# Kernel tuning notes

Hardware: AMD Instinct MI355X
Metric: run time of the kernel (lower is better)

Reference implementation:

```python
import jax, jax.numpy as jnp
import numpy as np

DIM, NHEADS = 1536, 12
HEAD_DIM = DIM // NHEADS  # 128

def _rope_params(max_pos, d):
    inv = 1.0 / (10000.0 ** (np.arange(0, d, 2, dtype=np.float64) / d))
    ang = np.outer(np.arange(max_pos, dtype=np.float64), inv)
    return np.stack([np.cos(ang), np.sin(ang)], -1).astype(np.float32)  # [max_pos, d//2, 2]

def setup_inputs() -> dict:
    key = jax.random.key(0)
    ks = jax.random.split(key, 8)
    B, F, H, W = 1, 3, 30, 52
    L = F * H * W  # 4680
    def w(k):
        return jax.random.normal(k, (DIM, DIM), jnp.float32) * 0.02
    # Wan rope table: head_dim=128 -> segments of real dim 44, 42, 42 (complex 22,21,21)
    freqs = np.concatenate([_rope_params(1024, 44), _rope_params(1024, 42), _rope_params(1024, 42)], axis=1)
    return {
        "x": jax.random.normal(ks[0], (B, L, DIM), jnp.float32),
        "wq": w(ks[1]), "bq": jnp.zeros((DIM,), jnp.float32),
        "wk": w(ks[2]), "bk": jnp.zeros((DIM,), jnp.float32),
        "wv": w(ks[3]), "bv": jnp.zeros((DIM,), jnp.float32),
        "wo": w(ks[4]), "bo": jnp.zeros((DIM,), jnp.float32),
        "gq": jnp.ones((DIM,), jnp.float32),
        "gk": jnp.ones((DIM,), jnp.float32),
        "freqs": jnp.asarray(freqs),                       # [1024, 64, 2] (cos, sin)
        "seq_lens": jnp.array([L], jnp.int64),
        "grid_sizes": jnp.array([[F, H, W]], jnp.int64),
        "F": F, "H": H, "W": W,
        "sink_size": 1, "local_attn_size": 2,
    }

def _rmsnorm(x, g, eps=1e-6):
    xf = x.astype(jnp.float32)
    return xf * jax.lax.rsqrt(jnp.mean(xf * xf, -1, keepdims=True) + eps) * g

def _rope_table(freqs, F, H, W):
    # freqs: [1024, 64, 2]; split complex dims [22, 21, 21] for (t, h, w)
    c = freqs.shape[1]
    s0 = c - 2 * (c // 3)          # 22
    s1 = c // 3                    # 21
    ft = jnp.broadcast_to(freqs[:F, :s0].reshape(F, 1, 1, s0, 2), (F, H, W, s0, 2))
    fh = jnp.broadcast_to(freqs[:H, s0:s0 + s1].reshape(1, H, 1, s1, 2), (F, H, W, s1, 2))
    fw = jnp.broadcast_to(freqs[:W, s0 + s1:].reshape(1, 1, W, s1, 2), (F, H, W, s1, 2))
    return jnp.concatenate([ft, fh, fw], -2).reshape(F * H * W, c, 2)  # [L, c, 2]

def _apply_rope(t, fr):
    # t: [B, L, n, d]; fr: [L, c, 2] with c = d // 2; complex multiply in real arithmetic
    B, L, n, d = t.shape
    c = d // 2
    tr = t.reshape(B, L, n, c, 2)
    a, b = tr[..., 0], tr[..., 1]
    cos = fr[None, :, None, :, 0]
    sin = fr[None, :, None, :, 1]
    out = jnp.stack([a * cos - b * sin, a * sin + b * cos], -1)
    return out.reshape(B, L, n, d)

def reference(x, wq, bq, wk, bk, wv, bv, wo, bo, gq, gk, freqs, seq_lens, grid_sizes,
              F, H, W, sink_size, local_attn_size):
    B, L, dim = x.shape
    n, d = NHEADS, HEAD_DIM
    q = _rmsnorm(x @ wq.T + bq, gq).reshape(B, L, n, d)
    k = _rmsnorm(x @ wk.T + bk, gk).reshape(B, L, n, d)
    v = (x @ wv.T + bv).reshape(B, L, n, d)
    fr = _rope_table(freqs, F, H, W)
    rq = _apply_rope(q, fr)
    rk = _apply_rope(k, fr)
    # sink + causal local-window block mask at frame granularity
    frame = jnp.arange(L) // (H * W)
    fq, fk = frame[:, None], frame[None, :]
    allow = (fk <= fq) & ((fk < sink_size) | (fq - fk < local_attn_size))  # [L, L]
    scores = jnp.einsum('blnd,bmnd->bnlm', rq, rk) / jnp.sqrt(jnp.float32(d))
    scores = jnp.where(allow[None, None], scores, -jnp.inf)
    p = jax.nn.softmax(scores, axis=-1)
    out = jnp.einsum('bnlm,bmnd->blnd', p, v).reshape(B, L, dim)
    return out @ wo.T + bo
```

## Files before the change

### kernel.cpp

```cpp
#include <hip/hip_runtime.h>

#define L_SEQ 4680
#define DIMSZ 1536
#define NHEAD 12
#define HDIM 128
#define FRAME 1560
#define NKT_ALL 74
#define SCALE_L2E 0.12751743f
#define WSZ 2359296
#define XSZ 7274496
#define PMPITCH 4736

typedef float f32x4 __attribute__((ext_vector_type(4)));
typedef _Float16 f16;
typedef _Float16 f16x2 __attribute__((ext_vector_type(2)));
typedef _Float16 f16x4 __attribute__((ext_vector_type(4)));
typedef _Float16 f16x8 __attribute__((ext_vector_type(8)));
typedef unsigned short u16;

__device__ __forceinline__ void gll16(const void* g, void* l) {
  __builtin_amdgcn_global_load_lds(
      (const __attribute__((address_space(1))) unsigned int*)g,
      (__attribute__((address_space(3))) unsigned int*)l, 16, 0, 0);
}

__global__ __launch_bounds__(256) void split_all(
    const float* __restrict__ x,  const float* __restrict__ wq,
    const float* __restrict__ wk, const float* __restrict__ wv,
    const float* __restrict__ wo, f16* __restrict__ xs,
    f16* __restrict__ whi) {
  const int kt = blockIdx.x;
  const int y = blockIdx.y;
  const float* src; f16* dst; int R, rt;
  if (y < 37) { src = x; dst = xs; R = L_SEQ; rt = y; }
  else {
    int i = y - 37;
    int z = i / 12; rt = i - z * 12; R = DIMSZ;
    src = z == 0 ? wq : (z == 1 ? wk : (z == 2 ? wv : wo));
    dst = whi + (size_t)z * WSZ;
  }
  const int t = threadIdx.x;
  const int row = t >> 1, c0 = (t & 1) * 16;
  const int gr = min(rt * 128 + row, R - 1);
  const float* s = &src[(size_t)gr * DIMSZ + kt * 32 + c0];
  float f[16];
#pragma unroll
  for (int i = 0; i < 4; ++i) *(float4*)&f[i * 4] = *(const float4*)&s[i * 4];
  size_t obase = ((size_t)(rt * 48 + kt)) * 4096 + row * 32;
#pragma unroll
  for (int cc = 0; cc < 2; ++cc) {
    f16x8 o;
#pragma unroll
    for (int i = 0; i < 8; ++i) o[i] = (f16)f[cc * 8 + i];
    int sl = (c0 >> 3) + cc;
    *(f16x8*)&dst[obase + ((sl * 8) ^ ((row & 3) * 8))] = o;
  }
}

__global__ __launch_bounds__(256, 3) void gemm_f16_1p(
    const f16* __restrict__ A, const f16* __restrict__ Wh,
    const float* __restrict__ b0, const float* __restrict__ b1, const float* __restrict__ b2,
    float* __restrict__ C, int M) {
  __shared__ f16 SA[8192];
  __shared__ f16 SW[8192];
  const int t = threadIdx.x;
  const int lane = t & 63, w = t >> 6;
  const int g = lane >> 4, ln = lane & 15;
  const int wm = w >> 1, wn = w & 1;
  const int mt = blockIdx.x, nt = blockIdx.y;
  const int which = nt / 12, ntw = nt - which * 12;
  const float* bias = which == 0 ? b0 : (which == 1 ? b1 : b2);
  const f16* srcA = A + (size_t)mt * 48 * 4096;
  const f16* srcW = Wh + ((size_t)which * 12 + ntw) * 48 * 4096;
  float* Cw = C + (size_t)which * ((size_t)L_SEQ * DIMSZ);
  f32x4 acc[4][4] = {};
  for (int kt2 = 0; kt2 < 24; ++kt2) {
    __syncthreads();
    size_t ko = (size_t)kt2 * 8192;
#pragma unroll
    for (int i = 0; i < 4; ++i) {
      gll16(srcA + ko + (i * 256 + t) * 8, &SA[(i * 256 + t) * 8]);
      gll16(srcW + ko + (i * 256 + t) * 8, &SW[(i * 256 + t) * 8]);
    }
    __syncthreads();
#pragma unroll
    for (int kc = 0; kc < 2; ++kc) {
      f16x8 af[4], wh4[4];
#pragma unroll
      for (int mi = 0; mi < 4; ++mi) {
        int row = wm * 64 + mi * 16 + ln;
        af[mi] = *(const f16x8*)&SA[kc * 4096 + row * 32 + ((g * 8) ^ ((row & 3) * 8))];
      }
#pragma unroll
      for (int ni = 0; ni < 4; ++ni) {
        int row = wn * 64 + ni * 16 + ln;
        wh4[ni] = *(const f16x8*)&SW[kc * 4096 + row * 32 + ((g * 8) ^ ((row & 3) * 8))];
      }
      __builtin_amdgcn_s_setprio(1);
#pragma unroll
      for (int mi = 0; mi < 4; ++mi)
#pragma unroll
        for (int ni = 0; ni < 4; ++ni)
          acc[mi][ni] = __builtin_amdgcn_mfma_f32_16x16x32_f16(af[mi], wh4[ni], acc[mi][ni], 0, 0, 0);
      __builtin_amdgcn_s_setprio(0);
    }
  }
#pragma unroll
  for (int mi = 0; mi < 4; ++mi)
#pragma unroll
    for (int ni = 0; ni < 4; ++ni) {
      int col = ntw * 128 + wn * 64 + ni * 16 + ln;
      float bv = bias[col];
#pragma unroll
      for (int r = 0; r < 4; ++r) {
        int row = mt * 128 + wm * 64 + mi * 16 + 4 * g + r;
        if (row < M) Cw[(size_t)row * DIMSZ + col] = acc[mi][ni][r] + bv;
      }
    }
}

__global__ __launch_bounds__(256) void norm_rope(
    const float* __restrict__ qf, const float* __restrict__ kf,
    const float* __restrict__ gq, const float* __restrict__ gk,
    const float* __restrict__ freqs, f16* __restrict__ q16, f16* __restrict__ k16) {
  const int pos = blockIdx.x;
  const bool isq = blockIdx.y == 0;
  const float* row = (isq ? qf : kf) + (size_t)pos * DIMSZ;
  const float* g = isq ? gq : gk;
  const int t = threadIdx.x;
  float2 ab[3];
  float ss = 0.f;
#pragma unroll
  for (int i = 0; i < 3; ++i) {
    ab[i] = *(const float2*)&row[2 * (t + 256 * i)];
    ss += ab[i].x * ab[i].x + ab[i].y * ab[i].y;
  }
#pragma unroll
  for (int m = 32; m; m >>= 1) ss += __shfl_xor(ss, m);
  __shared__ float part[4];
  if ((t & 63) == 0) part[t >> 6] = ss;
  __syncthreads();
  const float tot = part[0] + part[1] + part[2] + part[3];
  float scale = rsqrtf(tot * (1.f / DIMSZ) + 1e-6f);
  if (isq) scale *= SCALE_L2E;
  const int f = pos / FRAME;
  const int rem = pos - f * FRAME;
  const int hh = rem / 52;
  const int ww = rem - hh * 52;
  const int kt = pos >> 6, kk = pos & 63;
#pragma unroll
  for (int i = 0; i < 3; ++i) {
    const int p = t + 256 * i;
    const int c = p & 63;
    const int h = p >> 6;
    const int pr = c < 22 ? f : (c < 43 ? hh : ww);
    const float cs = freqs[(pr * 64 + c) * 2 + 0];
    const float sn = freqs[(pr * 64 + c) * 2 + 1];
    const float a = ab[i].x * scale * g[2 * p];
    const float b = ab[i].y * scale * g[2 * p + 1];
    f16x2 o;
    o[0] = (f16)(a * cs - b * sn);
    o[1] = (f16)(a * sn + b * cs);
    if (isq) {
      *(f16x2*)&q16[(size_t)pos * DIMSZ + 2 * p] = o;
    } else {
      const int s = c >> 2;
      size_t base = ((size_t)(h * NKT_ALL + kt)) << 13;
      *(f16x2*)&k16[base + kk * 128 + ((s * 8) ^ ((kk & 7) * 8)) + (c & 3) * 2] = o;
    }
  }
}

__global__ __launch_bounds__(256) void vconvert(const float* __restrict__ v, f16* __restrict__ v16) {
  __shared__ f16 Ls[64][136];
  const int kt = blockIdx.x, h = blockIdx.y, t = threadIdx.x;
#pragma unroll
  for (int p = 0; p < 8; ++p) {
    int e = p * 1024 + t * 4;
    int kk = e >> 7, d = e & 127;
    int gr = kt * 64 + kk;
    float4 val = make_float4(0.f, 0.f, 0.f, 0.f);
    if (gr < L_SEQ) val = *(const float4*)&v[(size_t)gr * DIMSZ + h * HDIM + d];
    f16x4 o;
    o[0] = (f16)val.x; o[1] = (f16)val.y; o[2] = (f16)val.z; o[3] = (f16)val.w;
    *(f16x4*)&Ls[kk][d] = o;
  }
  __syncthreads();
  f16* out = v16 + (((size_t)(h * NKT_ALL + kt)) << 13);
#pragma unroll
  for (int p = 0; p < 4; ++p) {
    int idx = p * 256 + t;
    int d = idx >> 3, c = idx & 7;
    const int nbb = (c & 1) * 2;
    const int g4 = (c >> 1) * 4;
    f16x8 o;
#pragma unroll
    for (int i = 0; i < 8; ++i) o[i] = Ls[(nbb + (i >> 2)) * 16 + g4 + (i & 3)][d];
    *(f16x8*)&out[d * 64 + 8 * (c ^ (d & 7))] = o;
  }
}

__global__ __launch_bounds__(256, 2) void attn_split(
    const f16* __restrict__ q16, const f16* __restrict__ k16,
    const f16* __restrict__ v16, float* __restrict__ pO,
    float* __restrict__ pm, float* __restrict__ pl) {
  __shared__ f16 Ks[2][8192];
  __shared__ f16 Vt[8192];
  __shared__ float Os[4][16][20];
  const int b = blockIdx.x;
  const int qt = 36 - b / 24;
  const int rem = b % 24;
  const int s = rem / 12;
  const int h = rem % 12;
  const int q0 = qt * 128;
  const int t = threadIdx.x;
  const int lane = t & 63, w = t >> 6;
  const int g = lane >> 4, ln = lane & 15;

  f16x8 qa[2][4];
  int klim[2];
  float m_run[2], l_run[2];
#pragma unroll
  for (int mi = 0; mi < 2; ++mi) {
    int qrow = min(q0 + w * 32 + mi * 16 + ln, L_SEQ - 1);
    klim[mi] = (qrow / FRAME + 1) * FRAME;
    m_run[mi] = -1e30f;
    l_run[mi] = 0.f;
    const f16* qb = &q16[(size_t)qrow * DIMSZ + h * HDIM + g * 8];
#pragma unroll
    for (int kc = 0; kc < 4; ++kc) qa[mi][kc] = *(const f16x8*)&qb[kc * 32];
  }
  const int klim0 = __shfl(klim[0], 0);
  f32x4 acc[2][8] = {};

  const int rmax = min(q0 + 127, L_SEQ - 1);
  const int nkt = ((rmax / FRAME + 1) * FRAME + 63) >> 6;
  const size_t hbase = ((size_t)h * NKT_ALL) << 13;

  f16x8 vv0, vv1, vv2, vv3;
  {
    const f16* tv = v16 + hbase + ((size_t)s << 13) + t * 8;
    vv0 = *(const f16x8*)(tv);
    vv1 = *(const f16x8*)(tv + 2048);
    vv2 = *(const f16x8*)(tv + 4096);
    vv3 = *(const f16x8*)(tv + 6144);
    f16* lv = Vt + t * 8;
    *(f16x8*)(lv) = vv0;
    *(f16x8*)(lv + 2048) = vv1;
    *(f16x8*)(lv + 4096) = vv2;
    *(f16x8*)(lv + 6144) = vv3;
    const f16* tk = k16 + hbase + ((size_t)s << 13);
#pragma unroll
    for (int i = 0; i < 4; ++i) gll16(tk + (i * 256 + t) * 8, &Ks[0][(i * 256 + t) * 8]);
  }
  int cur = 0;
  for (int kt = s; kt < nkt; kt += 2) {
    __syncthreads();
    const bool more = (kt + 2 < nkt);
    if (more) {
      size_t tb = hbase + ((size_t)(kt + 2) << 13);
      const f16* tk = k16 + tb;
#pragma unroll
      for (int i = 0; i < 4; ++i) gll16(tk + (i * 256 + t) * 8, &Ks[cur ^ 1][(i * 256 + t) * 8]);
      const f16* tv = v16 + tb + t * 8;
      vv0 = *(const f16x8*)(tv);
      vv1 = *(const f16x8*)(tv + 2048);
      vv2 = *(const f16x8*)(tv + 4096);
      vv3 = *(const f16x8*)(tv + 6144);
    }
    const f16* Kb = Ks[cur];

    f32x4 st[2][4] = {};
    __builtin_amdgcn_s_setprio(1);
#pragma unroll
    for (int nb = 0; nb < 4; ++nb) {
      int row = nb * 16 + ln;
#pragma unroll
      for (int kc = 0; kc < 4; ++kc) {
        f16x8 kb = *(const f16x8*)&Kb[row * 128 + ((g * 8 + kc * 32) ^ ((row & 7) * 8))];
        st[0][nb] = __builtin_amdgcn_mfma_f32_16x16x32_f16(kb, qa[0][kc], st[0][nb], 0, 0, 0);
        st[1][nb] = __builtin_amdgcn_mfma_f32_16x16x32_f16(kb, qa[1][kc], st[1][nb], 0, 0, 0);
      }
    }
    __builtin_amdgcn_s_setprio(0);

    f16x4 pb[2][4];
    const bool boundary = (kt * 64 + 64 > klim0);
#pragma unroll
    for (int mi = 0; mi < 2; ++mi) {
      float rm = -1e30f;
      if (boundary) {
#pragma unroll
        for (int nb = 0; nb < 4; ++nb)
#pragma unroll
          for (int r = 0; r < 4; ++r) {
            int key = kt * 64 + nb * 16 + 4 * g + r;
            float val = st[mi][nb][r];
            if (key >= klim[mi]) val = -1e30f;
            st[mi][nb][r] = val;
            rm = fmaxf(rm, val);
          }
      } else {
#pragma unroll
        for (int nb = 0; nb < 4; ++nb)
#pragma unroll
          for (int r = 0; r < 4; ++r) rm = fmaxf(rm, st[mi][nb][r]);
      }
      rm = fmaxf(rm, __shfl_xor(rm, 16));
      rm = fmaxf(rm, __shfl_xor(rm, 32));
      if (!__all(rm - m_run[mi] <= 8.0f)) {
        float mn = fmaxf(m_run[mi], rm);
        float fs = exp2f(m_run[mi] - mn);
        m_run[mi] = mn;
        l_run[mi] *= fs;
#pragma unroll
        for (int db = 0; db < 8; ++db)
#pragma unroll
          for (int r = 0; r < 4; ++r) acc[mi][db][r] *= fs;
      }
      float sm = 0.f;
#pragma unroll
      for (int nb = 0; nb < 4; ++nb)
#pragma unroll
        for (int r = 0; r < 4; ++r) {
          float e = exp2f(st[mi][nb][r] - m_run[mi]);
          sm += e;
          pb[mi][nb][r] = (f16)e;
        }
      sm += __shfl_xor(sm, 16);
      sm += __shfl_xor(sm, 32);
      l_run[mi] += sm;
    }

    __builtin_amdgcn_s_setprio(1);
#pragma unroll
    for (int db = 0; db < 8; ++db) {
      int d = db * 16 + ln;
#pragma unroll
      for (int nbp = 0; nbp < 2; ++nbp) {
        f16x8 vvv = *(const f16x8*)&Vt[d * 64 + 8 * ((g * 2 + nbp) ^ (d & 7))];
        f16x4 vlo = {vvv[0], vvv[1], vvv[2], vvv[3]};
        f16x4 vhi = {vvv[4], vvv[5], vvv[6], vvv[7]};
        acc[0][db] = __builtin_amdgcn_mfma_f32_16x16x16f16(vlo, pb[0][2 * nbp], acc[0][db], 0, 0, 0);
        acc[1][db] = __builtin_amdgcn_mfma_f32_16x16x16f16(vlo, pb[1][2 * nbp], acc[1][db], 0, 0, 0);
        acc[0][db] = __builtin_amdgcn_mfma_f32_16x16x16f16(vhi, pb[0][2 * nbp + 1], acc[0][db], 0, 0, 0);
        acc[1][db] = __builtin_amdgcn_mfma_f32_16x16x16f16(vhi, pb[1][2 * nbp + 1], acc[1][db], 0, 0, 0);
      }
    }
    __builtin_amdgcn_s_setprio(0);

    __syncthreads();
    if (more) {
      f16* lv = Vt + t * 8;
      *(f16x8*)(lv) = vv0;
      *(f16x8*)(lv + 2048) = vv1;
      *(f16x8*)(lv + 4096) = vv2;
      *(f16x8*)(lv + 6144) = vv3;
    }
    cur ^= 1;
  }

#pragma unroll
  for (int mi = 0; mi < 2; ++mi) {
    int qrow = q0 + w * 32 + mi * 16 + ln;
    if (g == 0) {
      pm[((size_t)s * 12 + h) * PMPITCH + qrow] = m_run[mi];
      pl[((size_t)s * 12 + h) * PMPITCH + qrow] = l_run[mi];
    }
#pragma unroll
    for (int db = 0; db < 8; ++db) {
      *(f32x4*)&Os[w][ln][4 * g] = acc[mi][db];
      asm volatile("s_waitcnt lgkmcnt(0)" ::: "memory");
#pragma unroll
      for (int r = 0; r < 4; ++r) {
        int q = q0 + w * 32 + mi * 16 + 4 * g + r;
        float val = Os[w][4 * g + r][ln];
        if (q < L_SEQ)
          pO[((size_t)s * L_SEQ + q) * DIMSZ + h * HDIM + db * 16 + ln] = val;
      }
      asm volatile("s_waitcnt lgkmcnt(0)" ::: "memory");
    }
  }
}

__global__ __launch_bounds__(256) void combine_k(
    const float* __restrict__ pO, const float* __restrict__ pm,
    const float* __restrict__ pl, f16* __restrict__ aos) {
  const int qt = blockIdx.x, h = blockIdx.y, t = threadIdx.x;
  const int row = t >> 1, d0 = (t & 1) * 64;
  const int q = min(qt * 128 + row, L_SEQ - 1);
  const float m0 = pm[(size_t)h * PMPITCH + q];
  const float m1 = pm[((size_t)12 + h) * PMPITCH + q];
  const float l0 = pl[(size_t)h * PMPITCH + q];
  const float l1 = pl[((size_t)12 + h) * PMPITCH + q];
  const float m = fmaxf(m0, m1);
  float w0 = exp2f(m0 - m), w1 = exp2f(m1 - m);
  const float rinv = 1.f / (w0 * l0 + w1 * l1);
  w0 *= rinv; w1 *= rinv;
  const float* o0 = &pO[(size_t)q * DIMSZ + h * HDIM + d0];
  const float* o1 = &pO[((size_t)L_SEQ + q) * DIMSZ + h * HDIM + d0];
  f16* outbase = aos + ((size_t)qt * 48 + h * 4) * 4096 + row * 32;
#pragma unroll
  for (int c8 = 0; c8 < 8; ++c8) {
    float a[8], bvals[8];
    *(float4*)&a[0] = *(const float4*)&o0[c8 * 8];
    *(float4*)&a[4] = *(const float4*)&o0[c8 * 8 + 4];
    *(float4*)&bvals[0] = *(const float4*)&o1[c8 * 8];
    *(float4*)&bvals[4] = *(const float4*)&o1[c8 * 8 + 4];
    f16x8 ov;
#pragma unroll
    for (int i = 0; i < 8; ++i) ov[i] = (f16)(w0 * a[i] + w1 * bvals[i]);
    int d = d0 + c8 * 8;
    int ktb = d >> 5;
    int s8 = (d & 31) >> 3;
    *(f16x8*)&outbase[(size_t)ktb * 4096 + ((s8 * 8) ^ ((row & 3) * 8))] = ov;
  }
}

extern "C" void kernel_launch(void* const* d_in, const int* in_sizes, int n_in,
                              void* d_out, int out_size, void* d_ws, size_t ws_size,
                              hipStream_t stream) {
  const float* x  = (const float*)d_in[0];
  const float* wq = (const float*)d_in[1];
  const float* bq = (const float*)d_in[2];
  const float* wk = (const float*)d_in[3];
  const float* bk = (const float*)d_in[4];
  const float* wv = (const float*)d_in[5];
  const float* bv = (const float*)d_in[6];
  const float* wo = (const float*)d_in[7];
  const float* bo = (const float*)d_in[8];
  const float* gq = (const float*)d_in[9];
  const float* gk = (const float*)d_in[10];
  const float* freqs = (const float*)d_in[11];
  float* out = (float*)d_out;
  float* ws = (float*)d_ws;

  const size_t LD = (size_t)L_SEQ * DIMSZ;

  float* qf = ws;
  float* kf = ws + LD;
  float* vf = ws + 2 * LD;
  f16* xs  = (f16*)(ws + 3 * LD);
  f16* k16 = xs + XSZ;
  f16* v16 = k16 + XSZ;
  f16* whi = v16 + XSZ;
  f16* q16 = xs;
  float* pO = qf;
  f16* aos = (f16*)vf;
  float* pm = vf + XSZ / 2;
  float* pl = pm + 2 * 12 * PMPITCH;
  f16* wo_hi = whi + 3 * (size_t)WSZ;

  dim3 blk(256);
  split_all<<<dim3(48, 85), blk, 0, stream>>>(x, wq, wk, wv, wo, xs, whi);
  gemm_f16_1p<<<dim3(37, 36), blk, 0, stream>>>(xs, whi, bq, bk, bv, qf, L_SEQ);
  norm_rope<<<dim3(L_SEQ, 2), blk, 0, stream>>>(qf, kf, gq, gk, freqs, q16, k16);
  vconvert<<<dim3(NKT_ALL, NHEAD), blk, 0, stream>>>(vf, v16);
  attn_split<<<dim3(37 * 24), blk, 0, stream>>>(q16, k16, v16, pO, pm, pl);
  combine_k<<<dim3(37, 12), blk, 0, stream>>>(pO, pm, pl, aos);
  gemm_f16_1p<<<dim3(37, 12), blk, 0, stream>>>(aos, wo_hi, bo, bo, bo, out, L_SEQ);
}
```

Before: 385.1 us.

## Emit fp16 QKV projections and merge norm-rope and V conversion into one kernel

The QKV GEMM now writes fp16 outputs instead of fp32, which halves the intermediate store and the reload by the norm/rope and V-transpose stage. norm_rope and vconvert are combined into a single launch with a 1D grid that switches on block index, removing one kernel launch. The workspace is re-laid out to fit the smaller buffers. Rounding Q/K to fp16 before RMSNorm adds a small precision risk, and the per-element fp16 stores in the GEMM epilogue are narrow writes.

```diff
diff --git a/kernel.cpp b/kernel.cpp
--- a/kernel.cpp
+++ b/kernel.cpp
@@ -10,6 +10,7 @@
 #define WSZ 2359296
 #define XSZ 7274496
 #define PMPITCH 4736
+#define LDSZ ((size_t)L_SEQ * DIMSZ)
 
 typedef float f32x4 __attribute__((ext_vector_type(4)));
 typedef _Float16 f16;
@@ -57,10 +58,11 @@
   }
 }
 
-__global__ __launch_bounds__(256, 3) void gemm_f16_1p(
+template <int OUT16>
+__global__ __launch_bounds__(256, 3) void gemm_f16_t(
     const f16* __restrict__ A, const f16* __restrict__ Wh,
     const float* __restrict__ b0, const float* __restrict__ b1, const float* __restrict__ b2,
-    float* __restrict__ C, int M) {
+    float* __restrict__ C, f16* __restrict__ C16, int M) {
   __shared__ f16 SA[8192];
   __shared__ f16 SW[8192];
   const int t = threadIdx.x;
@@ -72,7 +74,6 @@
   const float* bias = which == 0 ? b0 : (which == 1 ? b1 : b2);
   const f16* srcA = A + (size_t)mt * 48 * 4096;
   const f16* srcW = Wh + ((size_t)which * 12 + ntw) * 48 * 4096;
-  float* Cw = C + (size_t)which * ((size_t)L_SEQ * DIMSZ);
   f32x4 acc[4][4] = {};
   for (int kt2 = 0; kt2 < 24; ++kt2) {
     __syncthreads();
@@ -114,89 +115,96 @@
 #pragma unroll
       for (int r = 0; r < 4; ++r) {
         int row = mt * 128 + wm * 64 + mi * 16 + 4 * g + r;
-        if (row < M) Cw[(size_t)row * DIMSZ + col] = acc[mi][ni][r] + bv;
-      }
-    }
-}
-
-__global__ __launch_bounds__(256) void norm_rope(
-    const float* __restrict__ qf, const float* __restrict__ kf,
+        if (row < M) {
+          if (OUT16)
+            C16[(size_t)which * LDSZ + (size_t)row * DIMSZ + col] = (f16)(acc[mi][ni][r] + bv);
+          else
+            C[(size_t)which * LDSZ + (size_t)row * DIMSZ + col] = acc[mi][ni][r] + bv;
+        }
+      }
+    }
+}
+
+__global__ __launch_bounds__(256) void norm_v(
+    const f16* __restrict__ qh, const f16* __restrict__ kh,
     const float* __restrict__ gq, const float* __restrict__ gk,
-    const float* __restrict__ freqs, f16* __restrict__ q16, f16* __restrict__ k16) {
-  const int pos = blockIdx.x;
-  const bool isq = blockIdx.y == 0;
-  const float* row = (isq ? qf : kf) + (size_t)pos * DIMSZ;
-  const float* g = isq ? gq : gk;
+    const float* __restrict__ freqs, f16* __restrict__ q16, f16* __restrict__ k16,
+    const f16* __restrict__ vh, f16* __restrict__ v16) {
+  __shared__ f16 Ls[64][136];
+  __shared__ float part[4];
+  const int bx = blockIdx.x;
   const int t = threadIdx.x;
-  float2 ab[3];
-  float ss = 0.f;
-#pragma unroll
-  for (int i = 0; i < 3; ++i) {
-    ab[i] = *(const float2*)&row[2 * (t + 256 * i)];
-    ss += ab[i].x * ab[i].x + ab[i].y * ab[i].y;
-  }
-#pragma unroll
-  for (int m = 32; m; m >>= 1) ss += __shfl_xor(ss, m);
-  __shared__ float part[4];
-  if ((t & 63) == 0) part[t >> 6] = ss;
-  __syncthreads();
-  const float tot = part[0] + part[1] + part[2] + part[3];
-  float scale = rsqrtf(tot * (1.f / DIMSZ) + 1e-6f);
-  if (isq) scale *= SCALE_L2E;
-  const int f = pos / FRAME;
-  const int rem = pos - f * FRAME;
-  const int hh = rem / 52;
-  const int ww = rem - hh * 52;
-  const int kt = pos >> 6, kk = pos & 63;
-#pragma unroll
-  for (int i = 0; i < 3; ++i) {
-    const int p = t + 256 * i;
-    const int c = p & 63;
-    const int h = p >> 6;
-    const int pr = c < 22 ? f : (c < 43 ? hh : ww);
-    const float cs = freqs[(pr * 64 + c) * 2 + 0];
-    const float sn = freqs[(pr * 64 + c) * 2 + 1];
-    const float a = ab[i].x * scale * g[2 * p];
-    const float b = ab[i].y * scale * g[2 * p + 1];
-    f16x2 o;
-    o[0] = (f16)(a * cs - b * sn);
-    o[1] = (f16)(a * sn + b * cs);
-    if (isq) {
-      *(f16x2*)&q16[(size_t)pos * DIMSZ + 2 * p] = o;
-    } else {
-      const int s = c >> 2;
-      size_t base = ((size_t)(h * NKT_ALL + kt)) << 13;
-      *(f16x2*)&k16[base + kk * 128 + ((s * 8) ^ ((kk & 7) * 8)) + (c & 3) * 2] = o;
-    }
-  }
-}
-
-__global__ __launch_bounds__(256) void vconvert(const float* __restrict__ v, f16* __restrict__ v16) {
-  __shared__ f16 Ls[64][136];
-  const int kt = blockIdx.x, h = blockIdx.y, t = threadIdx.x;
-#pragma unroll
-  for (int p = 0; p < 8; ++p) {
-    int e = p * 1024 + t * 4;
-    int kk = e >> 7, d = e & 127;
-    int gr = kt * 64 + kk;
-    float4 val = make_float4(0.f, 0.f, 0.f, 0.f);
-    if (gr < L_SEQ) val = *(const float4*)&v[(size_t)gr * DIMSZ + h * HDIM + d];
-    f16x4 o;
-    o[0] = (f16)val.x; o[1] = (f16)val.y; o[2] = (f16)val.z; o[3] = (f16)val.w;
-    *(f16x4*)&Ls[kk][d] = o;
-  }
-  __syncthreads();
-  f16* out = v16 + (((size_t)(h * NKT_ALL + kt)) << 13);
-#pragma unroll
-  for (int p = 0; p < 4; ++p) {
-    int idx = p * 256 + t;
-    int d = idx >> 3, c = idx & 7;
-    const int nbb = (c & 1) * 2;
-    const int g4 = (c >> 1) * 4;
-    f16x8 o;
-#pragma unroll
-    for (int i = 0; i < 8; ++i) o[i] = Ls[(nbb + (i >> 2)) * 16 + g4 + (i & 3)][d];
-    *(f16x8*)&out[d * 64 + 8 * (c ^ (d & 7))] = o;
+  if (bx < 9360) {
+    const int pos = bx >> 1;
+    const bool isq = (bx & 1) == 0;
+    const f16* row = (isq ? qh : kh) + (size_t)pos * DIMSZ;
+    const float* g = isq ? gq : gk;
+    float2 ab[3];
+    float ss = 0.f;
+#pragma unroll
+    for (int i = 0; i < 3; ++i) {
+      f16x2 v = *(const f16x2*)&row[2 * (t + 256 * i)];
+      ab[i].x = (float)v[0];
+      ab[i].y = (float)v[1];
+      ss += ab[i].x * ab[i].x + ab[i].y * ab[i].y;
+    }
+#pragma unroll
+    for (int m = 32; m; m >>= 1) ss += __shfl_xor(ss, m);
+    if ((t & 63) == 0) part[t >> 6] = ss;
+    __syncthreads();
+    const float tot = part[0] + part[1] + part[2] + part[3];
+    float scale = rsqrtf(tot * (1.f / DIMSZ) + 1e-6f);
+    if (isq) scale *= SCALE_L2E;
+    const int f = pos / FRAME;
+    const int rem = pos - f * FRAME;
+    const int hh = rem / 52;
+    const int ww = rem - hh * 52;
+    const int kt = pos >> 6, kk = pos & 63;
+#pragma unroll
+    for (int i = 0; i < 3; ++i) {
+      const int p = t + 256 * i;
+      const int c = p & 63;
+      const int h = p >> 6;
+      const int pr = c < 22 ? f : (c < 43 ? hh : ww);
+      const float cs = freqs[(pr * 64 + c) * 2 + 0];
+      const float sn = freqs[(pr * 64 + c) * 2 + 1];
+      const float a = ab[i].x * scale * g[2 * p];
+      const float b = ab[i].y * scale * g[2 * p + 1];
+      f16x2 o;
+      o[0] = (f16)(a * cs - b * sn);
+      o[1] = (f16)(a * sn + b * cs);
+      if (isq) {
+        *(f16x2*)&q16[(size_t)pos * DIMSZ + 2 * p] = o;
+      } else {
+        const int s = c >> 2;
+        size_t base = ((size_t)(h * NKT_ALL + kt)) << 13;
+        *(f16x2*)&k16[base + kk * 128 + ((s * 8) ^ ((kk & 7) * 8)) + (c & 3) * 2] = o;
+      }
+    }
+  } else {
+    const int idx = bx - 9360;
+    const int kt = idx % NKT_ALL, h = idx / NKT_ALL;
+#pragma unroll
+    for (int p = 0; p < 8; ++p) {
+      int e = p * 1024 + t * 4;
+      int kk = e >> 7, d = e & 127;
+      int gr = min(kt * 64 + kk, L_SEQ - 1);
+      f16x4 o = *(const f16x4*)&vh[(size_t)gr * DIMSZ + h * HDIM + d];
+      *(f16x4*)&Ls[kk][d] = o;
+    }
+    __syncthreads();
+    f16* out = v16 + (((size_t)(h * NKT_ALL + kt)) << 13);
+#pragma unroll
+    for (int p = 0; p < 4; ++p) {
+      int idx2 = p * 256 + t;
+      int d = idx2 >> 3, c = idx2 & 7;
+      const int nbb = (c & 1) * 2;
+      const int g4 = (c >> 1) * 4;
+      f16x8 o;
+#pragma unroll
+      for (int i = 0; i < 8; ++i) o[i] = Ls[(nbb + (i >> 2)) * 16 + g4 + (i & 3)][d];
+      *(f16x8*)&out[d * 64 + 8 * (c ^ (d & 7))] = o;
+    }
   }
 }
 
@@ -435,28 +443,25 @@
   float* out = (float*)d_out;
   float* ws = (float*)d_ws;
 
-  const size_t LD = (size_t)L_SEQ * DIMSZ;
-
-  float* qf = ws;
-  float* kf = ws + LD;
-  float* vf = ws + 2 * LD;
-  f16* xs  = (f16*)(ws + 3 * LD);
+  float* pO = ws;
+  f16* qh = (f16*)ws;
+  f16* kh = qh + LDSZ;
+  f16* vh = kh + LDSZ;
+  f16* aos = (f16*)(ws + 2 * LDSZ);
+  float* pm = (float*)(aos + XSZ);
+  float* pl = pm + 2 * 12 * PMPITCH;
+  f16* xs  = (f16*)(pl + 2 * 12 * PMPITCH);
   f16* k16 = xs + XSZ;
   f16* v16 = k16 + XSZ;
   f16* whi = v16 + XSZ;
   f16* q16 = xs;
-  float* pO = qf;
-  f16* aos = (f16*)vf;
-  float* pm = vf + XSZ / 2;
-  float* pl = pm + 2 * 12 * PMPITCH;
   f16* wo_hi = whi + 3 * (size_t)WSZ;
 
   dim3 blk(256);
   split_all<<<dim3(48, 85), blk, 0, stream>>>(x, wq, wk, wv, wo, xs, whi);
-  gemm_f16_1p<<<dim3(37, 36), blk, 0, stream>>>(xs, whi, bq, bk, bv, qf, L_SEQ);
-  norm_rope<<<dim3(L_SEQ, 2), blk, 0, stream>>>(qf, kf, gq, gk, freqs, q16, k16);
-  vconvert<<<dim3(NKT_ALL, NHEAD), blk, 0, stream>>>(vf, v16);
+  gemm_f16_t<1><<<dim3(37, 36), blk, 0, stream>>>(xs, whi, bq, bk, bv, nullptr, qh, L_SEQ);
+  norm_v<<<dim3(9360 + 888), blk, 0, stream>>>(qh, kh, gq, gk, freqs, q16, k16, vh, v16);
   attn_split<<<dim3(37 * 24), blk, 0, stream>>>(q16, k16, v16, pO, pm, pl);
   combine_k<<<dim3(37, 12), blk, 0, stream>>>(pO, pm, pl, aos);
-  gemm_f16_1p<<<dim3(37, 12), blk, 0, stream>>>(aos, wo_hi, bo, bo, bo, out, L_SEQ);
-}
+  gemm_f16_t<0><<<dim3(37, 12), blk, 0, stream>>>(aos, wo_hi, bo, bo, bo, out, nullptr, L_SEQ);
+}
```

Result: faster. 370.5 us (-3.8%).
